# Performance work log

Measured on AMD Instinct MI355X. Metric: run time of the kernel, lower is better.

Reference implementation:

```python
import jax, jax.numpy as jnp
import numpy as np

POOL = (7, 7)
CANONICAL_SIZE = 224.0


def _crop_and_resize(feat, boxes, box_idx, pool):
    # feat: [B,H,W,C], boxes: [R,4] normalized (y1,x1,y2,x2), box_idx: [R] int32
    # Matches tf.image.crop_and_resize(method='bilinear', extrapolation_value=0).
    H, W = feat.shape[1], feat.shape[2]
    ph, pw = pool
    y1, x1, y2, x2 = boxes[:, 0], boxes[:, 1], boxes[:, 2], boxes[:, 3]
    fy = jnp.arange(ph, dtype=feat.dtype) / (ph - 1)
    fx = jnp.arange(pw, dtype=feat.dtype) / (pw - 1)
    in_y = (y1[:, None] + fy[None, :] * (y2 - y1)[:, None]) * (H - 1)  # [R,ph]
    in_x = (x1[:, None] + fx[None, :] * (x2 - x1)[:, None]) * (W - 1)  # [R,pw]
    y0 = jnp.floor(in_y)
    x0 = jnp.floor(in_x)
    wy = (in_y - y0)[:, :, None, None]   # [R,ph,1,1]
    wx = (in_x - x0)[:, None, :, None]   # [R,1,pw,1]
    y0i = y0.astype(jnp.int32)
    x0i = x0.astype(jnp.int32)
    y0c = jnp.clip(y0i, 0, H - 1)
    y1c = jnp.clip(y0i + 1, 0, H - 1)
    x0c = jnp.clip(x0i, 0, W - 1)
    x1c = jnp.clip(x0i + 1, 0, W - 1)
    b = box_idx[:, None, None]

    def g(yc, xc):  # gather [R,ph,pw,C]
        return feat[b, yc[:, :, None], xc[:, None, :], :]

    top = g(y0c, x0c) * (1 - wx) + g(y0c, x1c) * wx
    bot = g(y1c, x0c) * (1 - wx) + g(y1c, x1c) * wx
    out = top * (1 - wy) + bot * wy
    valid = ((in_y >= 0) & (in_y <= H - 1))[:, :, None] & \
            ((in_x >= 0) & (in_x <= W - 1))[:, None, :]
    return out * valid[..., None].astype(feat.dtype)


def reference(rois, image_h, image_w, p2, p3, p4, p5):
    feats = (p2, p3, p4, p5)  # FPN levels 2..5
    B, N, _ = rois.shape
    R = B * N
    boxes = rois.reshape(R, 4)
    box_idx = jnp.repeat(jnp.arange(B, dtype=jnp.int32), N)
    h = boxes[:, 2] - boxes[:, 0]
    w = boxes[:, 3] - boxes[:, 1]
    img_area = jnp.asarray(image_h * image_w, dtype=jnp.float32)
    # Mask R-CNN FPN level assignment: 4 + log2(sqrt(h*w)/(224/sqrt(image_area)))
    spec = jnp.log2(jnp.sqrt(jnp.maximum(h * w, 1e-12)) /
                    (CANONICAL_SIZE / jnp.sqrt(img_area)))
    roi_level = jnp.clip(4 + jnp.round(spec).astype(jnp.int32), 2, 5)  # [R]
    boxes_sg = jax.lax.stop_gradient(boxes)
    # Pool every roi against every level, then select its assigned level.
    pooled_l = jnp.stack([_crop_and_resize(f, boxes_sg, box_idx, POOL)
                          for f in feats])  # [4,R,ph,pw,C]
    pooled = pooled_l[roi_level - 2, jnp.arange(R)]  # [R,ph,pw,C]
    # Original concatenates level-by-level (stable within-level flat order).
    perm = jnp.argsort(roi_level)  # jnp.argsort is stable
    return pooled[perm]


def setup_inputs() -> dict:
    key = jax.random.key(0)
    ks = jax.random.split(key, 8)
    B, N, C = 2, 1000, 256
    bh = jax.random.uniform(ks[0], (B, N), minval=0.02, maxval=0.5)
    bw = jax.random.uniform(ks[1], (B, N), minval=0.02, maxval=0.5)
    y1 = jax.random.uniform(ks[2], (B, N)) * (1.0 - bh)
    x1 = jax.random.uniform(ks[3], (B, N)) * (1.0 - bw)
    rois = jnp.stack([y1, x1, y1 + bh, x1 + bw], axis=-1).astype(jnp.float32)
    return {
        'rois': rois,
        'image_h': 1024,
        'image_w': 1024,
        'p2': jax.random.normal(ks[4], (B, 256, 256, C), dtype=jnp.float32),
        'p3': jax.random.normal(ks[5], (B, 128, 128, C), dtype=jnp.float32),
        'p4': jax.random.normal(ks[6], (B, 64, 64, C), dtype=jnp.float32),
        'p5': jax.random.normal(ks[7], (B, 32, 32, C), dtype=jnp.float32),
    }
```

## Files before the change

### kernel.cpp

```cpp
#include <hip/hip_runtime.h>
#include <math.h>


#define MAX_R 2048
#define NCHUNK_MAX (MAX_R / 64)

typedef float f32x4 __attribute__((ext_vector_type(4)));

__global__ __launch_bounds__(1024)
void roi_setup_kernel(const float* __restrict__ rois,
                      const int* __restrict__ image_h,
                      const int* __restrict__ image_w,
                      int R,
                      int* __restrict__ level_out,
                      int* __restrict__ pos_out) {
    __shared__ int lvl_sh[MAX_R];
    __shared__ int wrank_sh[MAX_R];
    __shared__ int chunk_cnt[NCHUNK_MAX][4];
    __shared__ int chunk_base[NCHUNK_MAX][4];

    const int t    = threadIdx.x;
    const int lane = t & 63;
    const int wave = t >> 6;
    const int nwaves = blockDim.x >> 6;
    const int nchunk = (R + 63) / 64;

    const float canon = 224.0f / sqrtf((float)(image_h[0] * image_w[0]));

    for (int c = wave; c < nchunk; c += nwaves) {
        const int r = c * 64 + lane;
        int l = -1;
        if (r < R) {
            const float y1 = rois[r * 4 + 0];
            const float x1 = rois[r * 4 + 1];
            const float y2 = rois[r * 4 + 2];
            const float x2 = rois[r * 4 + 3];
            const float hw = (y2 - y1) * (x2 - x1);
            const float s = sqrtf(fmaxf(hw, 1e-12f));
            const double spec = log2((double)s / (double)canon);
            l = 4 + (int)rint(spec);
            l = min(5, max(2, l)) - 2;
            lvl_sh[r] = l;
        }
        unsigned long long m[4];
        #pragma unroll
        for (int i = 0; i < 4; ++i) m[i] = __ballot(l == i);
        if (r < R) {
            const unsigned long long below = (1ull << lane) - 1ull;
            wrank_sh[r] = __popcll(m[l] & below);
        }
        if (lane < 4) chunk_cnt[c][lane] = __popcll(m[lane]);
    }
    __syncthreads();

    if (t == 0) {
        int tot[4] = {0, 0, 0, 0};
        for (int c = 0; c < nchunk; ++c)
            for (int l = 0; l < 4; ++l) {
                chunk_base[c][l] = tot[l];
                tot[l] += chunk_cnt[c][l];
            }
        int base[4];
        int acc = 0;
        for (int l = 0; l < 4; ++l) { base[l] = acc; acc += tot[l]; }
        for (int c = 0; c < nchunk; ++c)
            for (int l = 0; l < 4; ++l) chunk_base[c][l] += base[l];
    }
    __syncthreads();

    for (int r = t; r < R; r += blockDim.x) {
        const int l = lvl_sh[r];
        level_out[r] = l;
        pos_out[r] = chunk_base[r >> 6][l] + wrank_sh[r];
    }
}

struct BinTask {
    const f32x4* f4;
    unsigned i00, i01, i10, i11, oidx;
    float wx, wy, vmask;
};

__device__ __forceinline__ BinTask make_task(int work, int N,
        const float* __restrict__ rois,
        const int* __restrict__ level,
        const int* __restrict__ pos,
        const float* __restrict__ p2, const float* __restrict__ p3,
        const float* __restrict__ p4, const float* __restrict__ p5,
        int lane) {
    BinTask T;
    const int r   = work / 49;
    const int bin = work - r * 49;
    const int py  = bin / 7;
    const int px  = bin - py * 7;
    const int b   = r / N;

    const int l = level[r];
    const float* feat;
    int H;
    switch (l) {
        case 0:  feat = p2; H = 256; break;
        case 1:  feat = p3; H = 128; break;
        case 2:  feat = p4; H = 64;  break;
        default: feat = p5; H = 32;  break;
    }
    const int W = H;

    const float y1 = rois[r * 4 + 0];
    const float x1 = rois[r * 4 + 1];
    const float y2 = rois[r * 4 + 2];
    const float x2 = rois[r * 4 + 3];

    const float fy = (float)py / 6.0f;
    const float fx = (float)px / 6.0f;
    const float in_y = (y1 + fy * (y2 - y1)) * (float)(H - 1);
    const float in_x = (x1 + fx * (x2 - x1)) * (float)(W - 1);

    const float y0f = floorf(in_y);
    const float x0f = floorf(in_x);
    T.wy = in_y - y0f;
    T.wx = in_x - x0f;
    const int y0i = (int)y0f;
    const int x0i = (int)x0f;
    const int y0c = min(H - 1, max(0, y0i));
    const int y1c = min(H - 1, max(0, y0i + 1));
    const int x0c = min(W - 1, max(0, x0i));
    const int x1c = min(W - 1, max(0, x0i + 1));

    T.vmask = (in_y >= 0.0f && in_y <= (float)(H - 1) &&
               in_x >= 0.0f && in_x <= (float)(W - 1)) ? 1.0f : 0.0f;

    T.f4 = (const f32x4*)feat;
    const unsigned bb = (unsigned)b * (unsigned)(H * W * 64);
    T.i00 = bb + (unsigned)(y0c * W + x0c) * 64u + (unsigned)lane;
    T.i01 = bb + (unsigned)(y0c * W + x1c) * 64u + (unsigned)lane;
    T.i10 = bb + (unsigned)(y1c * W + x0c) * 64u + (unsigned)lane;
    T.i11 = bb + (unsigned)(y1c * W + x1c) * 64u + (unsigned)lane;
    T.oidx = ((unsigned)pos[r] * 49u + (unsigned)bin) * 64u + (unsigned)lane;
    return T;
}

__device__ __forceinline__ f32x4 blend(f32x4 v00, f32x4 v01,
                                       f32x4 v10, f32x4 v11,
                                       float wx, float wy, float vmask) {
    const float omwx = 1.0f - wx;
    const float omwy = 1.0f - wy;
    const f32x4 top = v00 * omwx + v01 * wx;
    const f32x4 bot = v10 * omwx + v11 * wx;
    return (top * omwy + bot * wy) * vmask;
}

#define TASKS_PER_WAVE 4
#define TASKS_PER_BLOCK_ITER 16
#define BLOCK_ITERS 3
#define TASKS_PER_BLOCK (TASKS_PER_BLOCK_ITER * BLOCK_ITERS)

__global__ __launch_bounds__(256)
void roi_align_kernel(const float* __restrict__ rois,
                      const float* __restrict__ p2,
                      const float* __restrict__ p3,
                      const float* __restrict__ p4,
                      const float* __restrict__ p5,
                      const int* __restrict__ level,
                      const int* __restrict__ pos,
                      float* __restrict__ out,
                      int N, int total) {
    const int lane = threadIdx.x & 63;
    const int wv   = threadIdx.x >> 6;
    f32x4* __restrict__ o4 = (f32x4*)out;

    const int base = blockIdx.x * TASKS_PER_BLOCK;
    const int last = total - 1;

    for (int it = 0; it < BLOCK_ITERS; ++it) {
        const int t0 = base + it * TASKS_PER_BLOCK_ITER + wv * TASKS_PER_WAVE;
        if (t0 > last) return;

        BinTask T0 = make_task(min(t0 + 0, last), N, rois, level, pos, p2, p3, p4, p5, lane);
        BinTask T1 = make_task(min(t0 + 1, last), N, rois, level, pos, p2, p3, p4, p5, lane);
        BinTask T2 = make_task(min(t0 + 2, last), N, rois, level, pos, p2, p3, p4, p5, lane);
        BinTask T3 = make_task(min(t0 + 3, last), N, rois, level, pos, p2, p3, p4, p5, lane);

        const f32x4 a00 = T0.f4[T0.i00];
        const f32x4 a01 = T0.f4[T0.i01];
        const f32x4 a10 = T0.f4[T0.i10];
        const f32x4 a11 = T0.f4[T0.i11];
        const f32x4 b00 = T1.f4[T1.i00];
        const f32x4 b01 = T1.f4[T1.i01];
        const f32x4 b10 = T1.f4[T1.i10];
        const f32x4 b11 = T1.f4[T1.i11];
        const f32x4 c00 = T2.f4[T2.i00];
        const f32x4 c01 = T2.f4[T2.i01];
        const f32x4 c10 = T2.f4[T2.i10];
        const f32x4 c11 = T2.f4[T2.i11];
        const f32x4 d00 = T3.f4[T3.i00];
        const f32x4 d01 = T3.f4[T3.i01];
        const f32x4 d10 = T3.f4[T3.i10];
        const f32x4 d11 = T3.f4[T3.i11];

        __builtin_nontemporal_store(
            blend(a00, a01, a10, a11, T0.wx, T0.wy, T0.vmask), &o4[T0.oidx]);
        if (t0 + 1 <= last)
            __builtin_nontemporal_store(
                blend(b00, b01, b10, b11, T1.wx, T1.wy, T1.vmask), &o4[T1.oidx]);
        if (t0 + 2 <= last)
            __builtin_nontemporal_store(
                blend(c00, c01, c10, c11, T2.wx, T2.wy, T2.vmask), &o4[T2.oidx]);
        if (t0 + 3 <= last)
            __builtin_nontemporal_store(
                blend(d00, d01, d10, d11, T3.wx, T3.wy, T3.vmask), &o4[T3.oidx]);
    }
}

extern "C" void kernel_launch(void* const* d_in, const int* in_sizes, int n_in,
                              void* d_out, int out_size, void* d_ws, size_t ws_size,
                              hipStream_t stream) {
    const float* rois = (const float*)d_in[0];
    const int*   ih   = (const int*)d_in[1];
    const int*   iw   = (const int*)d_in[2];
    const float* p2   = (const float*)d_in[3];
    const float* p3   = (const float*)d_in[4];
    const float* p4   = (const float*)d_in[5];
    const float* p5   = (const float*)d_in[6];

    const int R = in_sizes[0] / 4;
    const int B = in_sizes[3] / (256 * 256 * 256);
    const int N = R / B;
    const int total = R * 49;

    int* level = (int*)d_ws;
    int* pos   = level + R;

    roi_setup_kernel<<<1, 1024, 0, stream>>>(rois, ih, iw, R, level, pos);

    const int blocks = (total + TASKS_PER_BLOCK - 1) / TASKS_PER_BLOCK;
    roi_align_kernel<<<blocks, 256, 0, stream>>>(rois, p2, p3, p4, p5,
                                                 level, pos, (float*)d_out, N, total);
}
```

Baseline: 269.6 us.

## Fuse ROI level/position setup into the align kernel, redundantly per block

Removes the separate single-block setup kernel and has every align block recompute all ROI levels and per-chunk ballot masks in shared memory, then derive the output positions of its own few ROIs. This removes one kernel launch and the serial single-block dependency, at the cost of redundant level computation (R ROIs) in every block. It also uses a float log2 with a double fallback near ties, doubles the tasks per block, and switches nontemporal stores to plain stores.

Measured after the change: 272.3 us. No clear change (+1.0%).

```diff
diff --git a/kernel.cpp b/kernel.cpp
--- a/kernel.cpp
+++ b/kernel.cpp
@@ -7,73 +7,10 @@
 
 typedef float f32x4 __attribute__((ext_vector_type(4)));
 
-__global__ __launch_bounds__(1024)
-void roi_setup_kernel(const float* __restrict__ rois,
-                      const int* __restrict__ image_h,
-                      const int* __restrict__ image_w,
-                      int R,
-                      int* __restrict__ level_out,
-                      int* __restrict__ pos_out) {
-    __shared__ int lvl_sh[MAX_R];
-    __shared__ int wrank_sh[MAX_R];
-    __shared__ int chunk_cnt[NCHUNK_MAX][4];
-    __shared__ int chunk_base[NCHUNK_MAX][4];
-
-    const int t    = threadIdx.x;
-    const int lane = t & 63;
-    const int wave = t >> 6;
-    const int nwaves = blockDim.x >> 6;
-    const int nchunk = (R + 63) / 64;
-
-    const float canon = 224.0f / sqrtf((float)(image_h[0] * image_w[0]));
-
-    for (int c = wave; c < nchunk; c += nwaves) {
-        const int r = c * 64 + lane;
-        int l = -1;
-        if (r < R) {
-            const float y1 = rois[r * 4 + 0];
-            const float x1 = rois[r * 4 + 1];
-            const float y2 = rois[r * 4 + 2];
-            const float x2 = rois[r * 4 + 3];
-            const float hw = (y2 - y1) * (x2 - x1);
-            const float s = sqrtf(fmaxf(hw, 1e-12f));
-            const double spec = log2((double)s / (double)canon);
-            l = 4 + (int)rint(spec);
-            l = min(5, max(2, l)) - 2;
-            lvl_sh[r] = l;
-        }
-        unsigned long long m[4];
-        #pragma unroll
-        for (int i = 0; i < 4; ++i) m[i] = __ballot(l == i);
-        if (r < R) {
-            const unsigned long long below = (1ull << lane) - 1ull;
-            wrank_sh[r] = __popcll(m[l] & below);
-        }
-        if (lane < 4) chunk_cnt[c][lane] = __popcll(m[lane]);
-    }
-    __syncthreads();
-
-    if (t == 0) {
-        int tot[4] = {0, 0, 0, 0};
-        for (int c = 0; c < nchunk; ++c)
-            for (int l = 0; l < 4; ++l) {
-                chunk_base[c][l] = tot[l];
-                tot[l] += chunk_cnt[c][l];
-            }
-        int base[4];
-        int acc = 0;
-        for (int l = 0; l < 4; ++l) { base[l] = acc; acc += tot[l]; }
-        for (int c = 0; c < nchunk; ++c)
-            for (int l = 0; l < 4; ++l) chunk_base[c][l] += base[l];
-    }
-    __syncthreads();
-
-    for (int r = t; r < R; r += blockDim.x) {
-        const int l = lvl_sh[r];
-        level_out[r] = l;
-        pos_out[r] = chunk_base[r >> 6][l] + wrank_sh[r];
-    }
-}
+#define TASKS_PER_WAVE 4
+#define WAVES_PER_BLOCK 4
+#define BLOCK_ITERS 6
+#define TASKS_PER_BLOCK (TASKS_PER_WAVE * WAVES_PER_BLOCK * BLOCK_ITERS)
 
 struct BinTask {
     const f32x4* f4;
@@ -81,10 +18,21 @@
     float wx, wy, vmask;
 };
 
-__device__ __forceinline__ BinTask make_task(int work, int N,
-        const float* __restrict__ rois,
-        const int* __restrict__ level,
-        const int* __restrict__ pos,
+__device__ __forceinline__ int roi_level_f(float y1, float x1, float y2, float x2,
+                                           float canon) {
+    const float hw = (y2 - y1) * (x2 - x1);
+    const float s = sqrtf(fmaxf(hw, 1e-12f));
+    const float spec = log2f(s / canon);
+    float rf = rintf(spec);
+    if (fabsf(fabsf(spec - rf) - 0.5f) < 1e-4f) {
+        rf = (float)rint(log2((double)s / (double)canon));
+    }
+    int l = 4 + (int)rf;
+    return min(5, max(2, l)) - 2;
+}
+
+__device__ __forceinline__ BinTask make_task(int work, int N, int rlo,
+        const int* lvl_loc, const int* pos_loc, const float* roi_loc,
         const float* __restrict__ p2, const float* __restrict__ p3,
         const float* __restrict__ p4, const float* __restrict__ p5,
         int lane) {
@@ -93,9 +41,15 @@
     const int bin = work - r * 49;
     const int py  = bin / 7;
     const int px  = bin - py * 7;
-    const int b   = r / N;
-
-    const int l = level[r];
+    const int b   = (int)((unsigned)r / (unsigned)N);
+
+    const int k = r - rlo;
+    const int l = lvl_loc[k];
+    const float y1 = roi_loc[k * 4 + 0];
+    const float x1 = roi_loc[k * 4 + 1];
+    const float y2 = roi_loc[k * 4 + 2];
+    const float x2 = roi_loc[k * 4 + 3];
+
     const float* feat;
     int H;
     switch (l) {
@@ -105,11 +59,6 @@
         default: feat = p5; H = 32;  break;
     }
     const int W = H;
-
-    const float y1 = rois[r * 4 + 0];
-    const float x1 = rois[r * 4 + 1];
-    const float y2 = rois[r * 4 + 2];
-    const float x2 = rois[r * 4 + 3];
 
     const float fy = (float)py / 6.0f;
     const float fx = (float)px / 6.0f;
@@ -136,7 +85,7 @@
     T.i01 = bb + (unsigned)(y0c * W + x1c) * 64u + (unsigned)lane;
     T.i10 = bb + (unsigned)(y1c * W + x0c) * 64u + (unsigned)lane;
     T.i11 = bb + (unsigned)(y1c * W + x1c) * 64u + (unsigned)lane;
-    T.oidx = ((unsigned)pos[r] * 49u + (unsigned)bin) * 64u + (unsigned)lane;
+    T.oidx = ((unsigned)pos_loc[k] * 49u + (unsigned)bin) * 64u + (unsigned)lane;
     return T;
 }
 
@@ -150,36 +99,98 @@
     return (top * omwy + bot * wy) * vmask;
 }
 
-#define TASKS_PER_WAVE 4
-#define TASKS_PER_BLOCK_ITER 16
-#define BLOCK_ITERS 3
-#define TASKS_PER_BLOCK (TASKS_PER_BLOCK_ITER * BLOCK_ITERS)
-
 __global__ __launch_bounds__(256)
-void roi_align_kernel(const float* __restrict__ rois,
-                      const float* __restrict__ p2,
-                      const float* __restrict__ p3,
-                      const float* __restrict__ p4,
-                      const float* __restrict__ p5,
-                      const int* __restrict__ level,
-                      const int* __restrict__ pos,
-                      float* __restrict__ out,
-                      int N, int total) {
-    const int lane = threadIdx.x & 63;
-    const int wv   = threadIdx.x >> 6;
+void roi_align_fused(const float* __restrict__ rois,
+                     const int* __restrict__ image_h,
+                     const int* __restrict__ image_w,
+                     const float* __restrict__ p2,
+                     const float* __restrict__ p3,
+                     const float* __restrict__ p4,
+                     const float* __restrict__ p5,
+                     float* __restrict__ out,
+                     int R, int N, int total) {
+    __shared__ unsigned long long masks_sh[NCHUNK_MAX][4];
+    __shared__ int cnt_sh[NCHUNK_MAX][4];
+    __shared__ int base_sh[NCHUNK_MAX][4];
+    __shared__ signed char lvl_sh[MAX_R];
+    __shared__ int lvl_loc[4];
+    __shared__ int pos_loc[4];
+    __shared__ float roi_loc[4 * 4];
+
+    const int t    = threadIdx.x;
+    const int lane = t & 63;
+    const int wv   = t >> 6;
+    const int nchunk = (R + 63) / 64;
+
+    const float canon = 224.0f / sqrtf((float)(image_h[0] * image_w[0]));
+
+    for (int c = wv; c < nchunk; c += WAVES_PER_BLOCK) {
+        const int r = c * 64 + lane;
+        int l = -1;
+        if (r < R) {
+            const float y1 = rois[r * 4 + 0];
+            const float x1 = rois[r * 4 + 1];
+            const float y2 = rois[r * 4 + 2];
+            const float x2 = rois[r * 4 + 3];
+            l = roi_level_f(y1, x1, y2, x2, canon);
+            lvl_sh[r] = (signed char)l;
+        }
+        unsigned long long m[4];
+        #pragma unroll
+        for (int i = 0; i < 4; ++i) m[i] = __ballot(l == i);
+        if (lane < 4) {
+            masks_sh[c][lane] = m[lane];
+            cnt_sh[c][lane]   = __popcll(m[lane]);
+        }
+    }
+    __syncthreads();
+
+    if (t == 0) {
+        int tot[4] = {0, 0, 0, 0};
+        for (int c = 0; c < nchunk; ++c)
+            for (int l = 0; l < 4; ++l) {
+                base_sh[c][l] = tot[l];
+                tot[l] += cnt_sh[c][l];
+            }
+        int base[4];
+        int acc = 0;
+        for (int l = 0; l < 4; ++l) { base[l] = acc; acc += tot[l]; }
+        for (int c = 0; c < nchunk; ++c)
+            for (int l = 0; l < 4; ++l) base_sh[c][l] += base[l];
+    }
+    __syncthreads();
+
+    const int task_base = blockIdx.x * TASKS_PER_BLOCK;
+    const int last = total - 1;
+    const int rlo = task_base / 49;
+    const int rhi = min(last, task_base + TASKS_PER_BLOCK - 1) / 49;
+    if (t <= rhi - rlo) {
+        const int r = rlo + t;
+        if (r < R) {
+            const int l = lvl_sh[r];
+            const int c = r >> 6;
+            const unsigned long long below = (1ull << (r & 63)) - 1ull;
+            lvl_loc[t] = l;
+            pos_loc[t] = base_sh[c][l] + __popcll(masks_sh[c][l] & below);
+            roi_loc[t * 4 + 0] = rois[r * 4 + 0];
+            roi_loc[t * 4 + 1] = rois[r * 4 + 1];
+            roi_loc[t * 4 + 2] = rois[r * 4 + 2];
+            roi_loc[t * 4 + 3] = rois[r * 4 + 3];
+        }
+    }
+    __syncthreads();
+
     f32x4* __restrict__ o4 = (f32x4*)out;
 
-    const int base = blockIdx.x * TASKS_PER_BLOCK;
-    const int last = total - 1;
-
     for (int it = 0; it < BLOCK_ITERS; ++it) {
-        const int t0 = base + it * TASKS_PER_BLOCK_ITER + wv * TASKS_PER_WAVE;
-        if (t0 > last) return;
-
-        BinTask T0 = make_task(min(t0 + 0, last), N, rois, level, pos, p2, p3, p4, p5, lane);
-        BinTask T1 = make_task(min(t0 + 1, last), N, rois, level, pos, p2, p3, p4, p5, lane);
-        BinTask T2 = make_task(min(t0 + 2, last), N, rois, level, pos, p2, p3, p4, p5, lane);
-        BinTask T3 = make_task(min(t0 + 3, last), N, rois, level, pos, p2, p3, p4, p5, lane);
+        const int t0 = task_base + it * (TASKS_PER_WAVE * WAVES_PER_BLOCK)
+                     + wv * TASKS_PER_WAVE;
+        if (t0 > last) break;
+
+        BinTask T0 = make_task(min(t0 + 0, last), N, rlo, lvl_loc, pos_loc, roi_loc, p2, p3, p4, p5, lane);
+        BinTask T1 = make_task(min(t0 + 1, last), N, rlo, lvl_loc, pos_loc, roi_loc, p2, p3, p4, p5, lane);
+        BinTask T2 = make_task(min(t0 + 2, last), N, rlo, lvl_loc, pos_loc, roi_loc, p2, p3, p4, p5, lane);
+        BinTask T3 = make_task(min(t0 + 3, last), N, rlo, lvl_loc, pos_loc, roi_loc, p2, p3, p4, p5, lane);
 
         const f32x4 a00 = T0.f4[T0.i00];
         const f32x4 a01 = T0.f4[T0.i01];
@@ -198,17 +209,13 @@
         const f32x4 d10 = T3.f4[T3.i10];
         const f32x4 d11 = T3.f4[T3.i11];
 
-        __builtin_nontemporal_store(
-            blend(a00, a01, a10, a11, T0.wx, T0.wy, T0.vmask), &o4[T0.oidx]);
+        o4[T0.oidx] = blend(a00, a01, a10, a11, T0.wx, T0.wy, T0.vmask);
         if (t0 + 1 <= last)
-            __builtin_nontemporal_store(
-                blend(b00, b01, b10, b11, T1.wx, T1.wy, T1.vmask), &o4[T1.oidx]);
+            o4[T1.oidx] = blend(b00, b01, b10, b11, T1.wx, T1.wy, T1.vmask);
         if (t0 + 2 <= last)
-            __builtin_nontemporal_store(
-                blend(c00, c01, c10, c11, T2.wx, T2.wy, T2.vmask), &o4[T2.oidx]);
+            o4[T2.oidx] = blend(c00, c01, c10, c11, T2.wx, T2.wy, T2.vmask);
         if (t0 + 3 <= last)
-            __builtin_nontemporal_store(
-                blend(d00, d01, d10, d11, T3.wx, T3.wy, T3.vmask), &o4[T3.oidx]);
+            o4[T3.oidx] = blend(d00, d01, d10, d11, T3.wx, T3.wy, T3.vmask);
     }
 }
 
@@ -228,12 +235,7 @@
     const int N = R / B;
     const int total = R * 49;
 
-    int* level = (int*)d_ws;
-    int* pos   = level + R;
-
-    roi_setup_kernel<<<1, 1024, 0, stream>>>(rois, ih, iw, R, level, pos);
-
     const int blocks = (total + TASKS_PER_BLOCK - 1) / TASKS_PER_BLOCK;
-    roi_align_kernel<<<blocks, 256, 0, stream>>>(rois, p2, p3, p4, p5,
-                                                 level, pos, (float*)d_out, N, total);
-}
+    roi_align_fused<<<blocks, 256, 0, stream>>>(rois, ih, iw, p2, p3, p4, p5,
+                                                (float*)d_out, R, N, total);
+}
```
